# Kernel tuning notes

Measured on AMD Instinct MI355X. Metric: run time of the kernel, lower is better.

The kernel has to match this reference:

```python
import jax, jax.numpy as jnp
import numpy as np

B, T, V = 512, 400, 32000
ENC, HID, EMB = 1024, 1024, 512


def setup_inputs() -> dict:
    key = jax.random.key(0)
    ks = jax.random.split(key, 10)
    vocab_dist = jax.random.uniform(ks[0], (B, V), dtype=jnp.float32)
    vocab_dist = vocab_dist / vocab_dist.sum(-1, keepdims=True)
    attn_dist = jax.random.uniform(ks[1], (B, T), dtype=jnp.float32)
    attn_dist = attn_dist / attn_dist.sum(-1, keepdims=True)
    return {
        "vocab_dist": vocab_dist,
        "attn_dist": attn_dist,
        "context": jax.random.normal(ks[2], (B, ENC), dtype=jnp.float32),
        "state": jax.random.normal(ks[3], (B, HID), dtype=jnp.float32),
        "emb": jax.random.normal(ks[4], (B, EMB), dtype=jnp.float32),
        "src_ids": jax.random.randint(ks[5], (B, T), 0, 32200),
        "vocab_size": V,
        # learned params: w_c: Linear(enc,1), w_s: Linear(hid,1), w_y: Linear(emb,1), bias b
        "w_c": jax.random.normal(ks[6], (ENC,), dtype=jnp.float32) / np.sqrt(ENC),
        "w_s": jax.random.normal(ks[7], (HID,), dtype=jnp.float32) / np.sqrt(HID),
        "w_y": jax.random.normal(ks[8], (EMB,), dtype=jnp.float32) / np.sqrt(EMB),
        "b": jnp.zeros((1,), dtype=jnp.float32),
    }


def reference(vocab_dist, attn_dist, context, state, emb, src_ids, vocab_size, w_c, w_s, w_y, b):
    # p_gen: [B, 1] gating scalar per batch row
    p_gen = jax.nn.sigmoid(
        (context @ w_c + state @ w_s + emb @ w_y)[:, None] + b
    )
    p_vocab = p_gen * vocab_dist                      # [B, V]
    p_copy = (1.0 - p_gen) * attn_dist                # [B, T]
    copy_mask = (src_ids < vocab_size).astype(p_copy.dtype)
    safe_src_ids = jnp.minimum(src_ids, vocab_size - 1)
    rows = jnp.arange(src_ids.shape[0])[:, None]      # [B, 1]
    final_dist = p_vocab.at[rows, safe_src_ids].add(p_copy * copy_mask)
    return final_dist
```

## Files before the change

kernel.cpp:

```cpp
#include <hip/hip_runtime.h>


#define CHUNK 8192

__global__ __launch_bounds__(256) void pg_gate_kernel(
    const float* __restrict__ context,
    const float* __restrict__ state,
    const float* __restrict__ emb,
    const float* __restrict__ w_c, const float* __restrict__ w_s,
    const float* __restrict__ w_y, const float* __restrict__ bias,
    float* __restrict__ pg,
    int ENC, int HID, int EMB)
{
    const int row = blockIdx.x;
    const int tid = threadIdx.x;
    float acc = 0.f;
    {
        const float4* a4 = (const float4*)(context + (size_t)row * ENC);
        const float4* w4 = (const float4*)w_c;
        for (int i = tid; i < (ENC >> 2); i += 256) {
            float4 a = a4[i], w = w4[i];
            acc += a.x * w.x + a.y * w.y + a.z * w.z + a.w * w.w;
        }
    }
    {
        const float4* a4 = (const float4*)(state + (size_t)row * HID);
        const float4* w4 = (const float4*)w_s;
        for (int i = tid; i < (HID >> 2); i += 256) {
            float4 a = a4[i], w = w4[i];
            acc += a.x * w.x + a.y * w.y + a.z * w.z + a.w * w.w;
        }
    }
    {
        const float4* a4 = (const float4*)(emb + (size_t)row * EMB);
        const float4* w4 = (const float4*)w_y;
        for (int i = tid; i < (EMB >> 2); i += 256) {
            float4 a = a4[i], w = w4[i];
            acc += a.x * w.x + a.y * w.y + a.z * w.z + a.w * w.w;
        }
    }
    #pragma unroll
    for (int off = 32; off > 0; off >>= 1)
        acc += __shfl_down(acc, off, 64);
    __shared__ float red[4];
    if ((tid & 63) == 0) red[tid >> 6] = acc;
    __syncthreads();
    if (tid == 0) {
        float s = red[0] + red[1] + red[2] + red[3] + bias[0];
        pg[row] = 1.f / (1.f + expf(-s));
    }
}

__global__ __launch_bounds__(256) void pg_scale_scatter_kernel(
    const float* __restrict__ vocab_dist,
    const float* __restrict__ attn_dist,
    const int*   __restrict__ src_ids,
    const int*   __restrict__ vocab_size_p,
    const float* __restrict__ pg,
    float* __restrict__ out,
    int T, int V)
{
    __shared__ float lds[CHUNK];
    const int row = blockIdx.y;
    const int v0  = blockIdx.x * CHUNK;
    const int len = min(CHUNK, V - v0);
    const int tid = threadIdx.x;

    float4* l4 = (float4*)lds;
    #pragma unroll 4
    for (int i = tid; i < (CHUNK >> 2); i += 256)
        l4[i] = make_float4(0.f, 0.f, 0.f, 0.f);

    const float p  = pg[row];
    const float pc = 1.f - p;
    const int   vs = *vocab_size_p;
    __syncthreads();

    const float* at = attn_dist + (size_t)row * T;
    const int*   si = src_ids  + (size_t)row * T;
    for (int t = tid; t < T; t += 256) {
        int id = si[t];
        if (id < vs) {
            int off = id - v0;
            if ((unsigned)off < (unsigned)len)
                atomicAdd(&lds[off], pc * at[t]);
        }
    }
    __syncthreads();

    const size_t base = (size_t)row * V + v0;
    const float4* vd4 = (const float4*)(vocab_dist + base);
    float4*       o4  = (float4*)(out + base);
    const int n4 = len >> 2;
    for (int i = tid; i < n4; i += 256) {
        float4 v = vd4[i];
        float4 a = l4[i];
        v.x = v.x * p + a.x;
        v.y = v.y * p + a.y;
        v.z = v.z * p + a.z;
        v.w = v.w * p + a.w;
        o4[i] = v;
    }
    for (int i = (n4 << 2) + tid; i < len; i += 256)
        out[base + i] = vocab_dist[base + i] * p + lds[i];
}

extern "C" void kernel_launch(void* const* d_in, const int* in_sizes, int n_in,
                              void* d_out, int out_size, void* d_ws, size_t ws_size,
                              hipStream_t stream) {
    const float* vocab_dist = (const float*)d_in[0];
    const float* attn_dist  = (const float*)d_in[1];
    const float* context    = (const float*)d_in[2];
    const float* state      = (const float*)d_in[3];
    const float* emb        = (const float*)d_in[4];
    const int*   src_ids    = (const int*)d_in[5];
    const int*   vocab_sz   = (const int*)d_in[6];
    const float* w_c        = (const float*)d_in[7];
    const float* w_s        = (const float*)d_in[8];
    const float* w_y        = (const float*)d_in[9];
    const float* bias       = (const float*)d_in[10];
    float* out = (float*)d_out;
    float* pg  = (float*)d_ws;

    const int ENC = in_sizes[7];
    const int HID = in_sizes[8];
    const int EMB = in_sizes[9];
    const int B   = in_sizes[2] / ENC;
    const int T   = in_sizes[1] / B;
    const int V   = in_sizes[0] / B;

    pg_gate_kernel<<<B, 256, 0, stream>>>(context, state, emb,
                                          w_c, w_s, w_y, bias, pg,
                                          ENC, HID, EMB);

    dim3 g2((V + CHUNK - 1) / CHUNK, B);
    pg_scale_scatter_kernel<<<g2, 256, 0, stream>>>(
        vocab_dist, attn_dist, src_ids, vocab_sz, pg, out, T, V);
}
```

Baseline: 139.8 us.

## Fuse gate computation into scatter kernel and use nontemporal vocab loads/stores

Folds the per-row sigmoid gate dot products into the scale/scatter kernel, so each chunk block recomputes the gate for its row. This removes one kernel launch and the workspace round trip. In exchange the context/state/emb reads are repeated for every chunk of a row (4x redundant). The main streaming loop now uses nontemporal loads and stores on vector types, aiming to cut cache pollution on the large vocab read and output write.

```diff
diff --git a/kernel.cpp b/kernel.cpp
--- a/kernel.cpp
+++ b/kernel.cpp
@@ -3,62 +3,20 @@
 
 #define CHUNK 8192
 
-__global__ __launch_bounds__(256) void pg_gate_kernel(
+typedef float f4 __attribute__((ext_vector_type(4)));
+
+__global__ __launch_bounds__(256) void pg_fused_kernel(
+    const float* __restrict__ vocab_dist,
+    const float* __restrict__ attn_dist,
+    const int*   __restrict__ src_ids,
+    const int*   __restrict__ vocab_size_p,
     const float* __restrict__ context,
     const float* __restrict__ state,
     const float* __restrict__ emb,
     const float* __restrict__ w_c, const float* __restrict__ w_s,
     const float* __restrict__ w_y, const float* __restrict__ bias,
-    float* __restrict__ pg,
-    int ENC, int HID, int EMB)
-{
-    const int row = blockIdx.x;
-    const int tid = threadIdx.x;
-    float acc = 0.f;
-    {
-        const float4* a4 = (const float4*)(context + (size_t)row * ENC);
-        const float4* w4 = (const float4*)w_c;
-        for (int i = tid; i < (ENC >> 2); i += 256) {
-            float4 a = a4[i], w = w4[i];
-            acc += a.x * w.x + a.y * w.y + a.z * w.z + a.w * w.w;
-        }
-    }
-    {
-        const float4* a4 = (const float4*)(state + (size_t)row * HID);
-        const float4* w4 = (const float4*)w_s;
-        for (int i = tid; i < (HID >> 2); i += 256) {
-            float4 a = a4[i], w = w4[i];
-            acc += a.x * w.x + a.y * w.y + a.z * w.z + a.w * w.w;
-        }
-    }
-    {
-        const float4* a4 = (const float4*)(emb + (size_t)row * EMB);
-        const float4* w4 = (const float4*)w_y;
-        for (int i = tid; i < (EMB >> 2); i += 256) {
-            float4 a = a4[i], w = w4[i];
-            acc += a.x * w.x + a.y * w.y + a.z * w.z + a.w * w.w;
-        }
-    }
-    #pragma unroll
-    for (int off = 32; off > 0; off >>= 1)
-        acc += __shfl_down(acc, off, 64);
-    __shared__ float red[4];
-    if ((tid & 63) == 0) red[tid >> 6] = acc;
-    __syncthreads();
-    if (tid == 0) {
-        float s = red[0] + red[1] + red[2] + red[3] + bias[0];
-        pg[row] = 1.f / (1.f + expf(-s));
-    }
-}
-
-__global__ __launch_bounds__(256) void pg_scale_scatter_kernel(
-    const float* __restrict__ vocab_dist,
-    const float* __restrict__ attn_dist,
-    const int*   __restrict__ src_ids,
-    const int*   __restrict__ vocab_size_p,
-    const float* __restrict__ pg,
     float* __restrict__ out,
-    int T, int V)
+    int T, int V, int ENC, int HID, int EMB)
 {
     __shared__ float lds[CHUNK];
     const int row = blockIdx.y;
@@ -66,18 +24,50 @@
     const int len = min(CHUNK, V - v0);
     const int tid = threadIdx.x;
 
-    float4* l4 = (float4*)lds;
+    float acc = 0.f;
+    {
+        const f4* a4 = (const f4*)(context + (size_t)row * ENC);
+        const f4* w4 = (const f4*)w_c;
+        for (int i = tid; i < (ENC >> 2); i += 256) {
+            f4 a = a4[i], w = w4[i];
+            acc += a.x * w.x + a.y * w.y + a.z * w.z + a.w * w.w;
+        }
+    }
+    {
+        const f4* a4 = (const f4*)(state + (size_t)row * HID);
+        const f4* w4 = (const f4*)w_s;
+        for (int i = tid; i < (HID >> 2); i += 256) {
+            f4 a = a4[i], w = w4[i];
+            acc += a.x * w.x + a.y * w.y + a.z * w.z + a.w * w.w;
+        }
+    }
+    {
+        const f4* a4 = (const f4*)(emb + (size_t)row * EMB);
+        const f4* w4 = (const f4*)w_y;
+        for (int i = tid; i < (EMB >> 2); i += 256) {
+            f4 a = a4[i], w = w4[i];
+            acc += a.x * w.x + a.y * w.y + a.z * w.z + a.w * w.w;
+        }
+    }
+    #pragma unroll
+    for (int off = 32; off > 0; off >>= 1)
+        acc += __shfl_down(acc, off, 64);
+    if ((tid & 63) == 0) lds[tid >> 6] = acc;
+    const int vs = *vocab_size_p;
+    __syncthreads();
+    const float s  = lds[0] + lds[1] + lds[2] + lds[3] + bias[0];
+    const float p  = 1.f / (1.f + expf(-s));
+    const float pc = 1.f - p;
+    __syncthreads();
+
+    f4* l4 = (f4*)lds;
     #pragma unroll 4
     for (int i = tid; i < (CHUNK >> 2); i += 256)
-        l4[i] = make_float4(0.f, 0.f, 0.f, 0.f);
-
-    const float p  = pg[row];
-    const float pc = 1.f - p;
-    const int   vs = *vocab_size_p;
+        l4[i] = (f4){0.f, 0.f, 0.f, 0.f};
     __syncthreads();
 
     const float* at = attn_dist + (size_t)row * T;
-    const int*   si = src_ids  + (size_t)row * T;
+    const int*   si = src_ids   + (size_t)row * T;
     for (int t = tid; t < T; t += 256) {
         int id = si[t];
         if (id < vs) {
@@ -89,17 +79,14 @@
     __syncthreads();
 
     const size_t base = (size_t)row * V + v0;
-    const float4* vd4 = (const float4*)(vocab_dist + base);
-    float4*       o4  = (float4*)(out + base);
+    const f4* vd4 = (const f4*)(vocab_dist + base);
+    f4*       o4  = (f4*)(out + base);
     const int n4 = len >> 2;
     for (int i = tid; i < n4; i += 256) {
-        float4 v = vd4[i];
-        float4 a = l4[i];
-        v.x = v.x * p + a.x;
-        v.y = v.y * p + a.y;
-        v.z = v.z * p + a.z;
-        v.w = v.w * p + a.w;
-        o4[i] = v;
+        f4 v = __builtin_nontemporal_load(vd4 + i);
+        f4 a = l4[i];
+        v = v * p + a;
+        __builtin_nontemporal_store(v, o4 + i);
     }
     for (int i = (n4 << 2) + tid; i < len; i += 256)
         out[base + i] = vocab_dist[base + i] * p + lds[i];
@@ -120,7 +107,6 @@
     const float* w_y        = (const float*)d_in[9];
     const float* bias       = (const float*)d_in[10];
     float* out = (float*)d_out;
-    float* pg  = (float*)d_ws;
 
     const int ENC = in_sizes[7];
     const int HID = in_sizes[8];
@@ -129,11 +115,9 @@
     const int T   = in_sizes[1] / B;
     const int V   = in_sizes[0] / B;
 
-    pg_gate_kernel<<<B, 256, 0, stream>>>(context, state, emb,
-                                          w_c, w_s, w_y, bias, pg,
-                                          ENC, HID, EMB);
-
-    dim3 g2((V + CHUNK - 1) / CHUNK, B);
-    pg_scale_scatter_kernel<<<g2, 256, 0, stream>>>(
-        vocab_dist, attn_dist, src_ids, vocab_sz, pg, out, T, V);
+    dim3 g((V + CHUNK - 1) / CHUNK, B);
+    pg_fused_kernel<<<g, 256, 0, stream>>>(
+        vocab_dist, attn_dist, src_ids, vocab_sz,
+        context, state, emb, w_c, w_s, w_y, bias,
+        out, T, V, ENC, HID, EMB);
 }
```

New measurement: 146.9 us. +5.1%, slower.
